# Kernel tuning notes

Measured on AMD Instinct MI355X. Metric: run time of the kernel, lower is better.

## Reference

```python
import jax, jax.numpy as jnp
import numpy as np

B, R, C, W, HEADS = 4, 32, 96, 4, 4
SHIFT = W // 2
N = W ** 3                      # tokens per window = 64
NW = (R // W) ** 3              # windows per sample = 512
MLP = 4 * C
EPS = 1e-5


def _build_attn_mask():
    img = np.zeros((R, R, R), dtype=np.float32)
    slices = (slice(0, -W), slice(-W, -SHIFT), slice(-SHIFT, None))
    cnt = 0
    for xs in slices:
        for ys in slices:
            for zs in slices:
                img[xs, ys, zs] = cnt
                cnt += 1
    m = img.reshape(R // W, W, R // W, W, R // W, W)
    m = m.transpose(0, 2, 4, 1, 3, 5).reshape(NW, N)          # (nW, N)
    diff = m[:, None, :] - m[:, :, None]                       # (nW, N, N)
    return np.where(diff != 0, -100.0, 0.0).astype(np.float32)


def setup_inputs() -> dict:
    key = jax.random.key(0)
    ks = jax.random.split(key, 8)
    s = 0.02
    return {
        "inputs": jax.random.normal(ks[0], (B, R ** 3, C), jnp.float32),
        "norm1_g": jnp.ones((C,), jnp.float32),
        "norm1_b": jnp.zeros((C,), jnp.float32),
        "qkv_w": jax.random.normal(ks[1], (C, 3 * C), jnp.float32) * s,
        "qkv_b": jnp.zeros((3 * C,), jnp.float32),
        "proj_w": jax.random.normal(ks[2], (C, C), jnp.float32) * s,
        "proj_b": jnp.zeros((C,), jnp.float32),
        "norm2_g": jnp.ones((C,), jnp.float32),
        "norm2_b": jnp.zeros((C,), jnp.float32),
        "mlp_w1": jax.random.normal(ks[3], (C, MLP), jnp.float32) * s,
        "mlp_b1": jnp.zeros((MLP,), jnp.float32),
        "mlp_w2": jax.random.normal(ks[4], (MLP, C), jnp.float32) * s,
        "mlp_b2": jnp.zeros((C,), jnp.float32),
        "attn_mask": jnp.asarray(_build_attn_mask()),
    }


def _layernorm(x, g, b):
    mu = jnp.mean(x, axis=-1, keepdims=True)
    var = jnp.mean(jnp.square(x - mu), axis=-1, keepdims=True)
    return (x - mu) * jax.lax.rsqrt(var + EPS) * g + b


def _box_partition(x):
    # (B, R, R, R, C) -> (B*nW, N, C)
    x = x.reshape(B, R // W, W, R // W, W, R // W, W, C)
    x = x.transpose(0, 1, 3, 5, 2, 4, 6, 7)
    return x.reshape(-1, N, C)


def _box_reverse(boxes):
    # (B*nW, N, C) -> (B, R, R, R, C)
    x = boxes.reshape(B, R // W, R // W, R // W, W, W, W, C)
    x = x.transpose(0, 1, 4, 2, 5, 3, 6, 7)
    return x.reshape(B, R, R, R, C)


def _forward(inputs, norm1_g, norm1_b, qkv_w, qkv_b, proj_w, proj_b,
             norm2_g, norm2_b, mlp_w1, mlp_b1, mlp_w2, mlp_b2, attn_mask):
    shortcut = inputs
    x = _layernorm(inputs, norm1_g, norm1_b)
    x = x.reshape(B, R, R, R, C)
    x = jnp.roll(x, shift=(-SHIFT, -SHIFT, -SHIFT), axis=(1, 2, 3))
    boxes = _box_partition(x)                                   # (B*nW, N, C)

    dh = C // HEADS
    qkv = boxes @ qkv_w + qkv_b                                 # (B*nW, N, 3C)
    qkv = qkv.reshape(-1, N, 3, HEADS, dh)
    q, k, v = qkv[:, :, 0], qkv[:, :, 1], qkv[:, :, 2]          # (B*nW, N, H, dh)
    scale = dh ** -0.5
    attn = jnp.einsum('wnhd,wmhd->whnm', q, k) * scale          # (B*nW, H, N, N)
    attn = attn.reshape(B, NW, HEADS, N, N) + attn_mask[None, :, None]
    attn = jax.nn.softmax(attn.reshape(-1, HEADS, N, N), axis=-1)
    out = jnp.einsum('whnm,wmhd->wnhd', attn, v).reshape(-1, N, C)
    out = out @ proj_w + proj_b                                 # (B*nW, N, C)

    x = _box_reverse(out)
    x = jnp.roll(x, shift=(SHIFT, SHIFT, SHIFT), axis=(1, 2, 3))
    x = x.reshape(B, R ** 3, C)
    x = x * 0.5 + shortcut                                      # drop_path=0 -> identity

    h = _layernorm(x, norm2_g, norm2_b)
    h = jax.nn.gelu(h @ mlp_w1 + mlp_b1) @ mlp_w2 + mlp_b2
    return h * 0.5 + x


def reference(inputs, norm1_g, norm1_b, qkv_w, qkv_b, proj_w, proj_b,
              norm2_g, norm2_b, mlp_w1, mlp_b1, mlp_w2, mlp_b2, attn_mask):
    return _forward(inputs, norm1_g, norm1_b, qkv_w, qkv_b, proj_w, proj_b,
                    norm2_g, norm2_b, mlp_w1, mlp_b1, mlp_w2, mlp_b2, attn_mask)
```

## Files before the change

### kernel.cpp

```cpp
#include <hip/hip_runtime.h>
#include <hip/hip_bf16.h>

#define CC 96
#define LDXP 104
#define KOFF 6656
#define XOFF 6656
#define KST 136
#define VST 72

typedef __bf16 bf16;
typedef __attribute__((ext_vector_type(8))) __bf16 bf16x8;
typedef __attribute__((ext_vector_type(4))) float f32x4;

#define MFMA16(a, b, c) __builtin_amdgcn_mfma_f32_16x16x32_bf16(a, b, c, 0, 0, 0)

__device__ __attribute__((aligned(16))) bf16 g_w1t[384 * 96];
__device__ __attribute__((aligned(16))) bf16 g_w2t[96 * 384];
__device__ __attribute__((aligned(16))) bf16 g_qkvwt[288 * 96];
__device__ __attribute__((aligned(16))) bf16 g_projwt[96 * 96];

template<bool BF>
__device__ __forceinline__ float ldg(const void* p, size_t i) {
    if constexpr (BF) return (float)((const bf16*)p)[i];
    else              return ((const float*)p)[i];
}

template<bool BF>
__device__ __forceinline__ void ld24(const void* p, size_t base, float* v) {
    if constexpr (BF) {
        const bf16* q = (const bf16*)p + base;
        #pragma unroll
        for (int i = 0; i < 3; i++) {
            bf16x8 f = *(const bf16x8*)(q + i * 8);
            #pragma unroll
            for (int j = 0; j < 8; j++) v[i * 8 + j] = (float)f[j];
        }
    } else {
        #pragma unroll
        for (int i = 0; i < 24; i++) v[i] = ((const float*)p)[base + i];
    }
}

__device__ __forceinline__ void st24_lds(bf16* dst, const float* v) {
    #pragma unroll
    for (int i = 0; i < 3; i++) {
        bf16x8 f;
        #pragma unroll
        for (int j = 0; j < 8; j++) f[j] = (bf16)v[i * 8 + j];
        *(bf16x8*)(dst + i * 8) = f;
    }
}

template<bool BF>
__device__ __forceinline__ void st24_glob(const bf16* stage, void* out, size_t g) {
    if constexpr (BF) {
        #pragma unroll
        for (int i = 0; i < 3; i++)
            *(bf16x8*)((bf16*)out + g + i * 8) = *(const bf16x8*)(stage + i * 8);
    } else {
        #pragma unroll
        for (int i = 0; i < 6; i++) {
            f32x4 v;
            #pragma unroll
            for (int j = 0; j < 4; j++) v[j] = (float)stage[i * 4 + j];
            *(f32x4*)((float*)out + g + i * 4) = v;
        }
    }
}

__device__ __forceinline__ bf16x8 ldsA(const bf16* base, int row0, int ld, int k0) {
    const int l = threadIdx.x & 63;
    return *(const bf16x8*)(base + (row0 + (l & 15)) * ld + k0 + (l >> 4) * 8);
}
__device__ __forceinline__ bf16x8 gB(const bf16* base, int n0, int K, int k0) {
    const int l = threadIdx.x & 63;
    return *(const bf16x8*)(base + (n0 + (l & 15)) * K + k0 + (l >> 4) * 8);
}

__device__ __forceinline__ float gelu_f(float x) {
    const float u = 1.5957691216057308f * (x + 0.044715f * x * x * x);
    return x - x / (__expf(u) + 1.0f);
}

template<bool BF>
__device__ void tbody(int idx, const void* qkv_w, const void* proj_w,
                      const void* w1, const void* w2) {
    if (idx < 384 * 96) {
        int n = idx / 96, k = idx % 96;
        g_w1t[idx] = (bf16)ldg<BF>(w1, (size_t)k * 384 + n);
    } else if (idx < 2 * 384 * 96) {
        int j = idx - 384 * 96; int n = j / 384, k = j % 384;
        g_w2t[j] = (bf16)ldg<BF>(w2, (size_t)k * 96 + n);
    } else if (idx < 2 * 384 * 96 + 288 * 96) {
        int j = idx - 2 * 384 * 96; int n = j / 96, k = j % 96;
        g_qkvwt[j] = (bf16)ldg<BF>(qkv_w, (size_t)k * 288 + n);
    } else {
        int j = idx - 2 * 384 * 96 - 288 * 96;
        if (j < 96 * 96) {
            int n = j / 96, k = j % 96;
            g_projwt[j] = (bf16)ldg<BF>(proj_w, (size_t)k * 96 + n);
        }
    }
}
__global__ __launch_bounds__(256) void transpose_kernel(
    const void* g1, const void* qkv_w, const void* proj_w, const void* w1, const void* w2) {
    const int idx = blockIdx.x * 256 + threadIdx.x;
    if (((const unsigned*)g1)[0] == 0x3F803F80u) tbody<true >(idx, qkv_w, proj_w, w1, w2);
    else                                         tbody<false>(idx, qkv_w, proj_w, w1, w2);
}

template<bool BF>
__device__ void fused_body(const void* x_in, const void* g1v, const void* b1v,
                           const void* qkv_b, const void* proj_b,
                           const void* g2v, const void* b2v, const void* mb1,
                           const void* mb2, void* out,
                           bf16* bufA, bf16* bufX, int* src_s)
{
    const int t = threadIdx.x;
    const int w = t >> 6;
    const int l = t & 63;
    const int box = blockIdx.x;
    const int b = box >> 9, bx = (box >> 6) & 7, by = (box >> 3) & 7, bz = box & 7;
    const bool b7x = (bx == 7), b7y = (by == 7), b7z = (bz == 7);
    const bool boundary = b7x || b7y || b7z;
    auto gc = [&](int n) -> int {
        return ((b7x && (n & 32)) ? 4 : 0) | ((b7y && (n & 8)) ? 2 : 0)
             | ((b7z && (n & 2)) ? 1 : 0);
    };
    const int qkvS = w * 4 + (w < 2 ? w : 2), qkvC = 5 - (w >> 1);
    const int sixS = w + (w < 2 ? w : 2),     sixC = 2 - (w >> 1);

    {
        const int row = t >> 2, hh = t & 3;
        *(f32x4*)(bufX + KOFF + row * KST + hh * 32 + 24) = (f32x4){0.f, 0.f, 0.f, 0.f};
        if (t < 64) *(f32x4*)(bufX + t * LDXP + 96) = (f32x4){0.f, 0.f, 0.f, 0.f};
    }

    {
        const int row = t >> 2, quad = t & 3;
        const int wx = row >> 4, wy = (row >> 2) & 3, wz = row & 3;
        const int sx = (bx * 4 + wx + 2) & 31;
        const int sy = (by * 4 + wy + 2) & 31;
        const int sz = (bz * 4 + wz + 2) & 31;
        const int src = ((b * 32 + sx) * 32 + sy) * 32 + sz;
        if (quad == 0) src_s[row] = src;
        float v[24];
        ld24<BF>(x_in, (size_t)src * CC + quad * 24, v);
        float s = 0.f, ss = 0.f;
        #pragma unroll
        for (int i = 0; i < 24; i++) { s += v[i]; ss += v[i] * v[i]; }
        s += __shfl_xor(s, 1);  ss += __shfl_xor(ss, 1);
        s += __shfl_xor(s, 2);  ss += __shfl_xor(ss, 2);
        const float mu = s * (1.f / 96.f);
        const float rstd = rsqrtf(ss * (1.f / 96.f) - mu * mu + 1e-5f);
        float o[24];
        #pragma unroll
        for (int i = 0; i < 24; i++) {
            const int c = quad * 24 + i;
            o[i] = (v[i] - mu) * rstd * ldg<BF>(g1v, c) + ldg<BF>(b1v, c);
        }
        st24_lds(bufA + row * LDXP + quad * 24, o);
    }
    __syncthreads();

    {
        bf16x8 aF[12];
        #pragma unroll
        for (int qt = 0; qt < 4; qt++)
            #pragma unroll
            for (int k = 0; k < 3; k++)
                aF[qt * 3 + k] = ldsA(bufA, qt * 16, LDXP, k * 32);
        __syncthreads();

        for (int i = 0; i < qkvC; i++) {
            const int nt = qkvS + i;
            const bf16x8 bB0 = gB(g_qkvwt, nt * 16, 96, 0);
            const bf16x8 bB1 = gB(g_qkvwt, nt * 16, 96, 32);
            const bf16x8 bB2 = gB(g_qkvwt, nt * 16, 96, 64);
            const int col = nt * 16 + (l & 15);
            const float bias = ldg<BF>(qkv_b, col);
            #pragma unroll
            for (int qt = 0; qt < 4; qt++) {
                f32x4 acc = {0.f, 0.f, 0.f, 0.f};
                acc = MFMA16(aF[qt * 3 + 0], bB0, acc);
                acc = MFMA16(aF[qt * 3 + 1], bB1, acc);
                acc = MFMA16(aF[qt * 3 + 2], bB2, acc);
                const int rq = qt * 16 + ((l >> 4) << 2);
                if (nt < 6) {
                    #pragma unroll
                    for (int r = 0; r < 4; r++)
                        bufX[(rq + r) * LDXP + col] = (bf16)(acc[r] + bias);
                } else if (nt < 12) {
                    const int c = col - 96, hh = c / 24, d = c - hh * 24;
                    #pragma unroll
                    for (int r = 0; r < 4; r++)
                        bufX[KOFF + (rq + r) * KST + hh * 32 + d] = (bf16)(acc[r] + bias);
                } else {
                    const int c = col - 192;
                    #pragma unroll
                    for (int r = 0; r < 4; r++)
                        bufA[c * VST + rq + r] = (bf16)(acc[r] + bias);
                }
            }
        }
    }
    __syncthreads();

    {
        const int h = w;
        bf16x8 aQ[4], bK[4], bV[2][2];
        #pragma unroll
        for (int qt = 0; qt < 4; qt++)
            aQ[qt] = *(const bf16x8*)(bufX + (qt * 16 + (l & 15)) * LDXP + h * 24 + ((l >> 4) << 3));
        #pragma unroll
        for (int mt = 0; mt < 4; mt++)
            bK[mt] = *(const bf16x8*)(bufX + KOFF + (mt * 16 + (l & 15)) * KST + h * 32 + ((l >> 4) << 3));
        #pragma unroll
        for (int ks = 0; ks < 2; ks++)
            #pragma unroll
            for (int nt = 0; nt < 2; nt++)
                bV[ks][nt] = *(const bf16x8*)(bufA + (h * 24 + nt * 8 + (l & 15)) * VST
                                              + ks * 32 + ((l >> 4) << 3));
        __syncthreads();

        f32x4 S[4][4];
        #pragma unroll
        for (int qt = 0; qt < 4; qt++)
            #pragma unroll
            for (int mt = 0; mt < 4; mt++)
                S[qt][mt] = MFMA16(aQ[qt], bK[mt], ((f32x4){0.f, 0.f, 0.f, 0.f}));

        const float scale = 0.20412414523193154f;
        bf16* pB = bufX + h * 4096;
        int gcol[4];
        if (boundary) {
            #pragma unroll
            for (int mt = 0; mt < 4; mt++) gcol[mt] = gc(mt * 16 + (l & 15));
        }
        #pragma unroll
        for (int qt = 0; qt < 4; qt++) {
            float e[4][4], rs[4] = {0.f, 0.f, 0.f, 0.f};
            if (boundary) {
                #pragma unroll
                for (int mt = 0; mt < 4; mt++)
                    #pragma unroll
                    for (int r = 0; r < 4; r++) {
                        const int row = qt * 16 + ((l >> 4) << 2) + r;
                        float ev = __expf(S[qt][mt][r] * scale);
                        ev = (gc(row) == gcol[mt]) ? ev : 0.f;
                        e[mt][r] = ev; rs[r] += ev;
                    }
            } else {
                #pragma unroll
                for (int mt = 0; mt < 4; mt++)
                    #pragma unroll
                    for (int r = 0; r < 4; r++) {
                        const float ev = __expf(S[qt][mt][r] * scale);
                        e[mt][r] = ev; rs[r] += ev;
                    }
            }
            #pragma unroll
            for (int r = 0; r < 4; r++) {
                rs[r] += __shfl_xor(rs[r], 1);
                rs[r] += __shfl_xor(rs[r], 2);
                rs[r] += __shfl_xor(rs[r], 4);
                rs[r] += __shfl_xor(rs[r], 8);
            }
            #pragma unroll
            for (int mt = 0; mt < 4; mt++) {
                const int colm = mt * 16 + (l & 15);
                const int chl = colm >> 3;
                #pragma unroll
                for (int r = 0; r < 4; r++) {
                    const int row = qt * 16 + ((l >> 4) << 2) + r;
                    const int ch = chl ^ (row & 7);
                    pB[row * 64 + ch * 8 + (colm & 7)] = (bf16)(e[mt][r] / rs[r]);
                }
            }
        }

        f32x4 O[4][2];
        #pragma unroll
        for (int qt = 0; qt < 4; qt++)
            #pragma unroll
            for (int nt = 0; nt < 2; nt++) O[qt][nt] = (f32x4){0.f, 0.f, 0.f, 0.f};
        #pragma unroll
        for (int ks = 0; ks < 2; ks++)
            #pragma unroll
            for (int qt = 0; qt < 4; qt++) {
                const int row = qt * 16 + (l & 15);
                const int ch = (ks * 4 + (l >> 4)) ^ (row & 7);
                const bf16x8 aP = *(const bf16x8*)(pB + row * 64 + ch * 8);
                O[qt][0] = MFMA16(aP, bV[ks][0], O[qt][0]);
                O[qt][1] = MFMA16(aP, bV[ks][1], O[qt][1]);
            }

        #pragma unroll
        for (int qt = 0; qt < 4; qt++)
            #pragma unroll
            for (int nt = 0; nt < 2; nt++) {
                const int cl = nt * 8 + (l & 15);
                if (nt == 0 || (l & 15) >= 8) {
                    #pragma unroll
                    for (int r = 0; r < 4; r++) {
                        const int row = qt * 16 + ((l >> 4) << 2) + r;
                        bufA[row * LDXP + h * 24 + cl] = (bf16)O[qt][nt][r];
                    }
                }
            }
    }
    __syncthreads();

    {
        bf16x8 pF[12];
        #pragma unroll
        for (int qt = 0; qt < 4; qt++)
            #pragma unroll
            for (int k = 0; k < 3; k++)
                pF[qt * 3 + k] = ldsA(bufA, qt * 16, LDXP, k * 32);
        __syncthreads();
        {
            const int row = t >> 2, quad = t & 3;
            float v[24];
            ld24<BF>(x_in, (size_t)src_s[row] * CC + quad * 24, v);
            st24_lds(bufA + row * LDXP + quad * 24, v);
        }
        __syncthreads();

        for (int i = 0; i < sixC; i++) {
            const int nt = sixS + i;
            const bf16x8 bB0 = gB(g_projwt, nt * 16, 96, 0);
            const bf16x8 bB1 = gB(g_projwt, nt * 16, 96, 32);
            const bf16x8 bB2 = gB(g_projwt, nt * 16, 96, 64);
            const int col = nt * 16 + (l & 15);
            const float bias = ldg<BF>(proj_b, col);
            #pragma unroll
            for (int qt = 0; qt < 4; qt++) {
                f32x4 acc = {0.f, 0.f, 0.f, 0.f};
                acc = MFMA16(pF[qt * 3 + 0], bB0, acc);
                acc = MFMA16(pF[qt * 3 + 1], bB1, acc);
                acc = MFMA16(pF[qt * 3 + 2], bB2, acc);
                const int rq = qt * 16 + ((l >> 4) << 2);
                #pragma unroll
                for (int r = 0; r < 4; r++) {
                    const float x2v = 0.5f * (acc[r] + bias)
                                    + (float)bufA[(rq + r) * LDXP + col];
                    bufX[XOFF + (rq + r) * LDXP + col] = (bf16)x2v;
                }
            }
        }
    }
    __syncthreads();

    {
        const int row = t >> 2, quad = t & 3;
        float v[24];
        #pragma unroll
        for (int i = 0; i < 3; i++) {
            bf16x8 f = *(const bf16x8*)(bufX + XOFF + row * LDXP + quad * 24 + i * 8);
            #pragma unroll
            for (int j = 0; j < 8; j++) v[i * 8 + j] = (float)f[j];
        }
        float s = 0.f, ss = 0.f;
        #pragma unroll
        for (int i = 0; i < 24; i++) { s += v[i]; ss += v[i] * v[i]; }
        s += __shfl_xor(s, 1);  ss += __shfl_xor(ss, 1);
        s += __shfl_xor(s, 2);  ss += __shfl_xor(ss, 2);
        const float mu = s * (1.f / 96.f);
        const float rstd = rsqrtf(ss * (1.f / 96.f) - mu * mu + 1e-5f);
        float o[24];
        #pragma unroll
        for (int i = 0; i < 24; i++) {
            const int c = quad * 24 + i;
            o[i] = (v[i] - mu) * rstd * ldg<BF>(g2v, c) + ldg<BF>(b2v, c);
        }
        st24_lds(bufX + row * LDXP + quad * 24, o);
    }
    __syncthreads();

    {
        bf16x8 mF[12];
        #pragma unroll
        for (int qt = 0; qt < 4; qt++)
            #pragma unroll
            for (int k = 0; k < 3; k++)
                mF[qt * 3 + k] = ldsA(bufX, qt * 16, LDXP, k * 32);

        f32x4 C[2][4];
        #pragma unroll
        for (int i = 0; i < 2; i++)
            #pragma unroll
            for (int qt = 0; qt < 4; qt++) C[i][qt] = (f32x4){0.f, 0.f, 0.f, 0.f};

        for (int c = 0; c < 4; c++) {
            if (c) __syncthreads();
            for (int i = 0; i < sixC; i++) {
                const int lt = sixS + i;
                const int n0 = c * 96 + lt * 16;
                const bf16x8 bB0 = gB(g_w1t, n0, 96, 0);
                const bf16x8 bB1 = gB(g_w1t, n0, 96, 32);
                const bf16x8 bB2 = gB(g_w1t, n0, 96, 64);
                const int colc = lt * 16 + (l & 15);
                const float bias = ldg<BF>(mb1, c * 96 + colc);
                #pragma unroll
                for (int qt = 0; qt < 4; qt++) {
                    f32x4 acc = {0.f, 0.f, 0.f, 0.f};
                    acc = MFMA16(mF[qt * 3 + 0], bB0, acc);
                    acc = MFMA16(mF[qt * 3 + 1], bB1, acc);
                    acc = MFMA16(mF[qt * 3 + 2], bB2, acc);
                    const int rq = qt * 16 + ((l >> 4) << 2);
                    #pragma unroll
                    for (int r = 0; r < 4; r++)
                        bufA[(rq + r) * LDXP + colc] = (bf16)gelu_f(acc[r] + bias);
                }
            }
            __syncthreads();
            for (int i = 0; i < sixC; i++) {
                const int ot = sixS + i;
                const bf16x8 bB0 = gB(g_w2t, ot * 16, 384, c * 96);
                const bf16x8 bB1 = gB(g_w2t, ot * 16, 384, c * 96 + 32);
                const bf16x8 bB2 = gB(g_w2t, ot * 16, 384, c * 96 + 64);
                #pragma unroll
                for (int qt = 0; qt < 4; qt++) {
                    const bf16x8 h0 = ldsA(bufA, qt * 16, LDXP, 0);
                    const bf16x8 h1 = ldsA(bufA, qt * 16, LDXP, 32);
                    const bf16x8 h2 = ldsA(bufA, qt * 16, LDXP, 64);
                    C[i][qt] = MFMA16(h0, bB0, C[i][qt]);
                    C[i][qt] = MFMA16(h1, bB1, C[i][qt]);
                    C[i][qt] = MFMA16(h2, bB2, C[i][qt]);
                }
            }
        }
        __syncthreads();

        for (int i = 0; i < sixC; i++) {
            const int ot = sixS + i;
            const int col = ot * 16 + (l & 15);
            const float bias = ldg<BF>(mb2, col);
            #pragma unroll
            for (int qt = 0; qt < 4; qt++) {
                const int rq = qt * 16 + ((l >> 4) << 2);
                #pragma unroll
                for (int r = 0; r < 4; r++) {
                    const float res = (float)bufX[XOFF + (rq + r) * LDXP + col];
                    bufA[(rq + r) * LDXP + col] = (bf16)(0.5f * (C[i][qt][r] + bias) + res);
                }
            }
        }
        __syncthreads();
        {
            const int row = t >> 2, quad = t & 3;
            st24_glob<BF>(bufA + row * LDXP + quad * 24, out,
                          (size_t)src_s[row] * CC + quad * 24);
        }
    }
}

__global__ __launch_bounds__(256, 3) void fused_kernel(
    const void* x_in, const void* g1, const void* b1, const void* qkv_b,
    const void* proj_b, const void* g2, const void* b2,
    const void* mb1, const void* mb2, void* out) {
    __shared__ bf16 bufA[6912];
    __shared__ bf16 bufX[16384];
    __shared__ int src_s[64];
    if (((const unsigned*)g1)[0] == 0x3F803F80u)
        fused_body<true >(x_in, g1, b1, qkv_b, proj_b, g2, b2, mb1, mb2, out,
                          bufA, bufX, src_s);
    else
        fused_body<false>(x_in, g1, b1, qkv_b, proj_b, g2, b2, mb1, mb2, out,
                          bufA, bufX, src_s);
}

extern "C" void kernel_launch(void* const* d_in, const int* in_sizes, int n_in,
                              void* d_out, int out_size, void* d_ws, size_t ws_size,
                              hipStream_t stream) {
    const void* x_in   = d_in[0];
    const void* g1     = d_in[1];
    const void* b1     = d_in[2];
    const void* qkv_w  = d_in[3];
    const void* qkv_b  = d_in[4];
    const void* proj_w = d_in[5];
    const void* proj_b = d_in[6];
    const void* g2     = d_in[7];
    const void* b2     = d_in[8];
    const void* w1     = d_in[9];
    const void* bias1  = d_in[10];
    const void* w2     = d_in[11];
    const void* bias2  = d_in[12];

    transpose_kernel<<<432, 256, 0, stream>>>(g1, qkv_w, proj_w, w1, w2);
    fused_kernel<<<2048, 256, 0, stream>>>(x_in, g1, b1, qkv_b, proj_b,
                                           g2, b2, bias1, bias2, d_out);
}
```

Before: 229.0 us.

## Split GEMM work as 2x2 row/column tiles per wave and fold 0.5 into weights

Each of the four waves now owns two 16-row query tiles and a contiguous half of the output column tiles, instead of all four row tiles and an uneven column slice. This balances MFMA work across waves and halves the A-fragment registers, and the MLP second GEMM loads its hidden fragments from LDS once per chunk instead of once per output tile. The 0.5 residual scaling is folded into the proj and w2 weights at transpose time and into the biases, removing a multiply per element. The trade-off is that each weight B fragment is now loaded by two waves rather than one, and the bf16 rounding of the pre-scaled weights changes slightly.

Result: no change. 230.1 us (+0.5%).

```diff
diff --git a/kernel.cpp b/kernel.cpp
--- a/kernel.cpp
+++ b/kernel.cpp
@@ -90,7 +90,7 @@
         g_w1t[idx] = (bf16)ldg<BF>(w1, (size_t)k * 384 + n);
     } else if (idx < 2 * 384 * 96) {
         int j = idx - 384 * 96; int n = j / 384, k = j % 384;
-        g_w2t[j] = (bf16)ldg<BF>(w2, (size_t)k * 96 + n);
+        g_w2t[j] = (bf16)(0.5f * ldg<BF>(w2, (size_t)k * 96 + n));
     } else if (idx < 2 * 384 * 96 + 288 * 96) {
         int j = idx - 2 * 384 * 96; int n = j / 96, k = j % 96;
         g_qkvwt[j] = (bf16)ldg<BF>(qkv_w, (size_t)k * 288 + n);
@@ -98,7 +98,7 @@
         int j = idx - 2 * 384 * 96 - 288 * 96;
         if (j < 96 * 96) {
             int n = j / 96, k = j % 96;
-            g_projwt[j] = (bf16)ldg<BF>(proj_w, (size_t)k * 96 + n);
+            g_projwt[j] = (bf16)(0.5f * ldg<BF>(proj_w, (size_t)k * 96 + n));
         }
     }
 }
@@ -127,8 +127,9 @@
         return ((b7x && (n & 32)) ? 4 : 0) | ((b7y && (n & 8)) ? 2 : 0)
              | ((b7z && (n & 2)) ? 1 : 0);
     };
-    const int qkvS = w * 4 + (w < 2 ? w : 2), qkvC = 5 - (w >> 1);
-    const int sixS = w + (w < 2 ? w : 2),     sixC = 2 - (w >> 1);
+    const int ntb18 = (w >> 1) * 9;
+    const int ntb6  = (w >> 1) * 3;
+    const int qtb   = (w & 1) * 2;
 
     {
         const int row = t >> 2, hh = t & 3;
@@ -164,28 +165,29 @@
     __syncthreads();
 
     {
-        bf16x8 aF[12];
-        #pragma unroll
-        for (int qt = 0; qt < 4; qt++)
+        bf16x8 aF[2][3];
+        #pragma unroll
+        for (int iq = 0; iq < 2; iq++)
             #pragma unroll
             for (int k = 0; k < 3; k++)
-                aF[qt * 3 + k] = ldsA(bufA, qt * 16, LDXP, k * 32);
+                aF[iq][k] = ldsA(bufA, (qtb + iq) * 16, LDXP, k * 32);
         __syncthreads();
 
-        for (int i = 0; i < qkvC; i++) {
-            const int nt = qkvS + i;
+        #pragma unroll 3
+        for (int i = 0; i < 9; i++) {
+            const int nt = ntb18 + i;
             const bf16x8 bB0 = gB(g_qkvwt, nt * 16, 96, 0);
             const bf16x8 bB1 = gB(g_qkvwt, nt * 16, 96, 32);
             const bf16x8 bB2 = gB(g_qkvwt, nt * 16, 96, 64);
             const int col = nt * 16 + (l & 15);
             const float bias = ldg<BF>(qkv_b, col);
             #pragma unroll
-            for (int qt = 0; qt < 4; qt++) {
+            for (int iq = 0; iq < 2; iq++) {
                 f32x4 acc = {0.f, 0.f, 0.f, 0.f};
-                acc = MFMA16(aF[qt * 3 + 0], bB0, acc);
-                acc = MFMA16(aF[qt * 3 + 1], bB1, acc);
-                acc = MFMA16(aF[qt * 3 + 2], bB2, acc);
-                const int rq = qt * 16 + ((l >> 4) << 2);
+                acc = MFMA16(aF[iq][0], bB0, acc);
+                acc = MFMA16(aF[iq][1], bB1, acc);
+                acc = MFMA16(aF[iq][2], bB2, acc);
+                const int rq = (qtb + iq) * 16 + ((l >> 4) << 2);
                 if (nt < 6) {
                     #pragma unroll
                     for (int r = 0; r < 4; r++)
@@ -312,12 +314,12 @@
     __syncthreads();
 
     {
-        bf16x8 pF[12];
-        #pragma unroll
-        for (int qt = 0; qt < 4; qt++)
+        bf16x8 pF[2][3];
+        #pragma unroll
+        for (int iq = 0; iq < 2; iq++)
             #pragma unroll
             for (int k = 0; k < 3; k++)
-                pF[qt * 3 + k] = ldsA(bufA, qt * 16, LDXP, k * 32);
+                pF[iq][k] = ldsA(bufA, (qtb + iq) * 16, LDXP, k * 32);
         __syncthreads();
         {
             const int row = t >> 2, quad = t & 3;
@@ -327,23 +329,24 @@
         }
         __syncthreads();
 
-        for (int i = 0; i < sixC; i++) {
-            const int nt = sixS + i;
+        #pragma unroll
+        for (int i = 0; i < 3; i++) {
+            const int nt = ntb6 + i;
             const bf16x8 bB0 = gB(g_projwt, nt * 16, 96, 0);
             const bf16x8 bB1 = gB(g_projwt, nt * 16, 96, 32);
             const bf16x8 bB2 = gB(g_projwt, nt * 16, 96, 64);
             const int col = nt * 16 + (l & 15);
-            const float bias = ldg<BF>(proj_b, col);
-            #pragma unroll
-            for (int qt = 0; qt < 4; qt++) {
+            const float bias = 0.5f * ldg<BF>(proj_b, col);
+            #pragma unroll
+            for (int iq = 0; iq < 2; iq++) {
                 f32x4 acc = {0.f, 0.f, 0.f, 0.f};
-                acc = MFMA16(pF[qt * 3 + 0], bB0, acc);
-                acc = MFMA16(pF[qt * 3 + 1], bB1, acc);
-                acc = MFMA16(pF[qt * 3 + 2], bB2, acc);
-                const int rq = qt * 16 + ((l >> 4) << 2);
+                acc = MFMA16(pF[iq][0], bB0, acc);
+                acc = MFMA16(pF[iq][1], bB1, acc);
+                acc = MFMA16(pF[iq][2], bB2, acc);
+                const int rq = (qtb + iq) * 16 + ((l >> 4) << 2);
                 #pragma unroll
                 for (int r = 0; r < 4; r++) {
-                    const float x2v = 0.5f * (acc[r] + bias)
+                    const float x2v = acc[r] + bias
                                     + (float)bufA[(rq + r) * LDXP + col];
                     bufX[XOFF + (rq + r) * LDXP + col] = (bf16)x2v;
                 }
@@ -379,23 +382,24 @@
     __syncthreads();
 
     {
-        bf16x8 mF[12];
-        #pragma unroll
-        for (int qt = 0; qt < 4; qt++)
+        bf16x8 mF[2][3];
+        #pragma unroll
+        for (int iq = 0; iq < 2; iq++)
             #pragma unroll
             for (int k = 0; k < 3; k++)
-                mF[qt * 3 + k] = ldsA(bufX, qt * 16, LDXP, k * 32);
-
-        f32x4 C[2][4];
-        #pragma unroll
-        for (int i = 0; i < 2; i++)
-            #pragma unroll
-            for (int qt = 0; qt < 4; qt++) C[i][qt] = (f32x4){0.f, 0.f, 0.f, 0.f};
+                mF[iq][k] = ldsA(bufX, (qtb + iq) * 16, LDXP, k * 32);
+
+        f32x4 C[3][2];
+        #pragma unroll
+        for (int i = 0; i < 3; i++)
+            #pragma unroll
+            for (int iq = 0; iq < 2; iq++) C[i][iq] = (f32x4){0.f, 0.f, 0.f, 0.f};
 
         for (int c = 0; c < 4; c++) {
             if (c) __syncthreads();
-            for (int i = 0; i < sixC; i++) {
-                const int lt = sixS + i;
+            #pragma unroll
+            for (int i = 0; i < 3; i++) {
+                const int lt = ntb6 + i;
                 const int n0 = c * 96 + lt * 16;
                 const bf16x8 bB0 = gB(g_w1t, n0, 96, 0);
                 const bf16x8 bB1 = gB(g_w1t, n0, 96, 32);
@@ -403,47 +407,52 @@
                 const int colc = lt * 16 + (l & 15);
                 const float bias = ldg<BF>(mb1, c * 96 + colc);
                 #pragma unroll
-                for (int qt = 0; qt < 4; qt++) {
+                for (int iq = 0; iq < 2; iq++) {
                     f32x4 acc = {0.f, 0.f, 0.f, 0.f};
-                    acc = MFMA16(mF[qt * 3 + 0], bB0, acc);
-                    acc = MFMA16(mF[qt * 3 + 1], bB1, acc);
-                    acc = MFMA16(mF[qt * 3 + 2], bB2, acc);
-                    const int rq = qt * 16 + ((l >> 4) << 2);
+                    acc = MFMA16(mF[iq][0], bB0, acc);
+                    acc = MFMA16(mF[iq][1], bB1, acc);
+                    acc = MFMA16(mF[iq][2], bB2, acc);
+                    const int rq = (qtb + iq) * 16 + ((l >> 4) << 2);
                     #pragma unroll
                     for (int r = 0; r < 4; r++)
                         bufA[(rq + r) * LDXP + colc] = (bf16)gelu_f(acc[r] + bias);
                 }
             }
             __syncthreads();
-            for (int i = 0; i < sixC; i++) {
-                const int ot = sixS + i;
+            bf16x8 hF[2][3];
+            #pragma unroll
+            for (int iq = 0; iq < 2; iq++)
+                #pragma unroll
+                for (int k = 0; k < 3; k++)
+                    hF[iq][k] = ldsA(bufA, (qtb + iq) * 16, LDXP, k * 32);
+            #pragma unroll
+            for (int i = 0; i < 3; i++) {
+                const int ot = ntb6 + i;
                 const bf16x8 bB0 = gB(g_w2t, ot * 16, 384, c * 96);
                 const bf16x8 bB1 = gB(g_w2t, ot * 16, 384, c * 96 + 32);
                 const bf16x8 bB2 = gB(g_w2t, ot * 16, 384, c * 96 + 64);
                 #pragma unroll
-                for (int qt = 0; qt < 4; qt++) {
-                    const bf16x8 h0 = ldsA(bufA, qt * 16, LDXP, 0);
-                    const bf16x8 h1 = ldsA(bufA, qt * 16, LDXP, 32);
-                    const bf16x8 h2 = ldsA(bufA, qt * 16, LDXP, 64);
-                    C[i][qt] = MFMA16(h0, bB0, C[i][qt]);
-                    C[i][qt] = MFMA16(h1, bB1, C[i][qt]);
-                    C[i][qt] = MFMA16(h2, bB2, C[i][qt]);
+                for (int iq = 0; iq < 2; iq++) {
+                    C[i][iq] = MFMA16(hF[iq][0], bB0, C[i][iq]);
+                    C[i][iq] = MFMA16(hF[iq][1], bB1, C[i][iq]);
+                    C[i][iq] = MFMA16(hF[iq][2], bB2, C[i][iq]);
                 }
             }
         }
         __syncthreads();
 
-        for (int i = 0; i < sixC; i++) {
-            const int ot = sixS + i;
+        #pragma unroll
+        for (int i = 0; i < 3; i++) {
+            const int ot = ntb6 + i;
             const int col = ot * 16 + (l & 15);
-            const float bias = ldg<BF>(mb2, col);
-            #pragma unroll
-            for (int qt = 0; qt < 4; qt++) {
-                const int rq = qt * 16 + ((l >> 4) << 2);
+            const float bias = 0.5f * ldg<BF>(mb2, col);
+            #pragma unroll
+            for (int iq = 0; iq < 2; iq++) {
+                const int rq = (qtb + iq) * 16 + ((l >> 4) << 2);
                 #pragma unroll
                 for (int r = 0; r < 4; r++) {
                     const float res = (float)bufX[XOFF + (rq + r) * LDXP + col];
-                    bufA[(rq + r) * LDXP + col] = (bf16)(0.5f * (C[i][qt][r] + bias) + res);
+                    bufA[(rq + r) * LDXP + col] = (bf16)(C[i][iq][r] + bias + res);
                 }
             }
         }
```
